# Performance work log

Measured on AMD Instinct MI355X. Metric: run time of the kernel, lower is better.

The kernel has to match this reference:

```python
import jax, jax.numpy as jnp
import numpy as np

B, C, H, W = 4, 64, 160, 160
COUT, K = 64, 3
STRIDE, PAD, DIL = 1, 1, 1


def setup_inputs() -> dict:
    key = jax.random.key(0)
    k1, k2, k3, k4, k5 = jax.random.split(key, 5)
    x = jax.random.normal(k1, (B, C, H, W), dtype=jnp.float32)
    # small offset-conv weights -> offsets of O(1) pixel, realistic sampling
    w_off = jax.random.normal(k2, (2 * K * K, C, K, K), dtype=jnp.float32) * 0.01
    b_off = jax.random.normal(k3, (2 * K * K,), dtype=jnp.float32) * 0.01
    weight = jax.random.normal(k4, (COUT, C, K, K), dtype=jnp.float32) / np.sqrt(C * K * K)
    bias = jax.random.normal(k5, (COUT,), dtype=jnp.float32) * 0.01
    return {"x": x, "w_off": w_off, "b_off": b_off, "weight": weight, "bias": bias}


def _deform_conv2d(x, offset, weight, bias):
    """torchvision-style deform_conv2d (v1, groups=1, offset_groups=1)."""
    b, c, h, w = x.shape
    cout, _, k, _ = weight.shape
    kk = k * k
    ho, wo = offset.shape[2], offset.shape[3]
    off = offset.reshape(b, kk, 2, ho, wo)
    dy, dx = off[:, :, 0], off[:, :, 1]  # [B,KK,Ho,Wo]
    # base sampling grid: p0 + kernel offset
    base_y = (jnp.arange(ho) * STRIDE - PAD)[None, :] + (jnp.arange(k) * DIL)[:, None]  # [K,Ho]
    base_x = (jnp.arange(wo) * STRIDE - PAD)[None, :] + (jnp.arange(k) * DIL)[:, None]  # [K,Wo]
    by = jnp.repeat(base_y, k, axis=0)   # [KK,Ho]  (k index = kh*K + kw)
    bx = jnp.tile(base_x, (k, 1))        # [KK,Wo]
    py = by[None, :, :, None] + dy       # [B,KK,Ho,Wo]
    px = bx[None, :, None, :] + dx
    y0 = jnp.floor(py)
    x0 = jnp.floor(px)
    ly = (py - y0)[:, None]              # [B,1,KK,Ho,Wo]
    lx = (px - x0)[:, None]
    y0i = y0.astype(jnp.int32)
    x0i = x0.astype(jnp.int32)
    x_flat = x.reshape(b, c, h * w)

    def gather(yi, xi):
        valid = (yi >= 0) & (yi < h) & (xi >= 0) & (xi < w)
        yc = jnp.clip(yi, 0, h - 1)
        xc = jnp.clip(xi, 0, w - 1)
        lin = (yc * w + xc).reshape(b, 1, -1)
        v = jnp.take_along_axis(x_flat, lin, axis=2).reshape(b, c, kk, ho, wo)
        return v * valid[:, None].astype(x.dtype)

    v00 = gather(y0i, x0i)
    v01 = gather(y0i, x0i + 1)
    v10 = gather(y0i + 1, x0i)
    v11 = gather(y0i + 1, x0i + 1)
    sampled = (v00 * (1 - ly) * (1 - lx) + v01 * (1 - ly) * lx
               + v10 * ly * (1 - lx) + v11 * ly * lx)  # [B,C,KK,Ho,Wo]
    out = jnp.einsum('bckhw,ock->bohw', sampled, weight.reshape(cout, c, kk))
    return out + bias[None, :, None, None]


def reference(x, w_off, b_off, weight, bias):
    offset = jax.lax.conv_general_dilated(
        x, w_off, (STRIDE, STRIDE), ((PAD, PAD), (PAD, PAD)),
        rhs_dilation=(DIL, DIL),
        dimension_numbers=('NCHW', 'OIHW', 'NCHW')) + b_off[None, :, None, None]
    return _deform_conv2d(x, offset, weight, bias)
```

## Files before the change

### kernel.cpp

```cpp
#include <hip/hip_runtime.h>
#include <hip/hip_bf16.h>

#define Bq   4
#define Cc   64
#define Hh   160
#define Ww   160
#define HWp  (Hh * Ww)
#define COUTc 64

typedef __attribute__((ext_vector_type(8))) _Float16 f16x8;
typedef __attribute__((ext_vector_type(4))) _Float16 f16x4;
typedef __attribute__((ext_vector_type(4))) float f32x4;
typedef __attribute__((ext_vector_type(2))) float f32x2;
typedef __attribute__((ext_vector_type(4))) int   int4v;

#define WTBF_SHORTS   (72 * 512)
#define WTOFFF_SHORTS (36 * 512)
#define XCL_OFS       (WTBF_SHORTS + WTOFFF_SHORTS)
#define XCL_PIX       ((size_t)Bq * HWp)
#define XCL_SHORTS    (XCL_PIX * 64 + 64)

#define HROWS 7
#define HCOLS 36
#define HPX   72
#define HSTR  (HCOLS * HPX)

__device__ __forceinline__ short f2h(float f) {
    union { _Float16 h; short s; } v; v.h = (_Float16)f; return v.s;
}
__device__ __forceinline__ unsigned pk2h(float a, float b) {
    union { _Float16 h[2]; unsigned u; } v;
    v.h[0] = (_Float16)a; v.h[1] = (_Float16)b; return v.u;
}
__device__ __forceinline__ f16x8 vsplat(_Float16 v) {
    return (f16x8){v, v, v, v, v, v, v, v};
}

__global__ __launch_bounds__(256) void prep_all(const float* __restrict__ x,
                                                const float* __restrict__ w,
                                                const float* __restrict__ w_off,
                                                short* __restrict__ ws) {
    int blk = blockIdx.x;
    int tid = threadIdx.x;
    if (blk < 400) {
        int g = blk * 256 + tid;
        int b = g / HWp, p = g - b * HWp;
        const float* xp = x + (size_t)b * Cc * HWp + p;
        short* op = ws + XCL_OFS + (size_t)g * 64;
#pragma unroll
        for (int cg = 0; cg < 8; ++cg) {
            unsigned d[4];
#pragma unroll
            for (int dj = 0; dj < 4; ++dj) {
                float f0 = xp[(size_t)(cg * 8 + 2 * dj) * HWp];
                float f1 = xp[(size_t)(cg * 8 + 2 * dj + 1) * HWp];
                d[dj] = pk2h(f0, f1);
            }
            *(int4v*)(op + cg * 8) = *(int4v*)d;
        }
    } else if (blk < 544) {
        int i = (blk - 400) * 256 + tid;
        if (i < WTBF_SHORTS) {
            int fidx = i >> 9, r = i & 511;
            int l = r >> 3, j = r & 7;
            int cg = fidx & 3, th = fidx >> 2;
            int tap = th >> 1, h = th & 1;
            int o = cg * 16 + (l & 15);
            int c = h * 32 + ((l >> 4) << 3) + j;
            ws[i] = f2h(w[o * 576 + c * 9 + tap]);
        }
        if (i < WTOFFF_SHORTS) {
            int fidx = i >> 9, r = i & 511;
            int l = r >> 3, j = r & 7;
            int g = fidx & 1, th = fidx >> 1;
            int tap = th >> 1, h = th & 1;
            int oc = g * 16 + (l & 15);
            int c = h * 32 + ((l >> 4) << 3) + j;
            float v = (oc < 18) ? w_off[oc * 576 + c * 9 + tap] : 0.f;
            ws[WTBF_SHORTS + i] = f2h(v);
        }
    } else {
        if (tid < 8)
            *(int4v*)((char*)(ws + XCL_OFS) + XCL_PIX * 128 + tid * 16) =
                (int4v){0, 0, 0, 0};
    }
}

__global__ __launch_bounds__(256, 3) void fused_cl(const short* __restrict__ ws,
                                                   const float* __restrict__ b_off,
                                                   const float* __restrict__ bias,
                                                   float* __restrict__ out) {
    __shared__ short halo_s[HROWS * HCOLS * HPX];
    __shared__ float offbuf[64][20];
    __shared__ int4v tapT[64][9];

    int tid = threadIdx.x;
    int wid = tid >> 6;
    int l   = tid & 63;
    int lr  = l & 15;
    int lg  = l >> 4;

    int bid = blockIdx.x;
    int g_blk = (bid & 7) * 200 + (bid >> 3);

    int b  = g_blk / 400;
    int r  = g_blk - b * 400;
    int ty2 = r / 5;
    int tx2 = r - ty2 * 5;
    int y  = ty2 * 2;
    int x0 = tx2 * 32;

    const short* wTbF   = ws;
    const short* wToffF = ws + WTBF_SHORTS;
    const char*  xclb   = (const char*)(ws + XCL_OFS) + (size_t)b * HWp * 128;

    for (int i = tid; i < HROWS * HCOLS * 8; i += 256) {
        int pl = i >> 3, cg2 = i & 7;
        int hy = pl / HCOLS, hx = pl - hy * HCOLS;
        int gy = y - 2 + hy, gx = x0 - 2 + hx;
        int4v v;
        if (gy >= 0 && gy < Hh && gx >= 0 && gx < Ww)
            v = *(const int4v*)(xclb + (size_t)(gy * Ww + gx) * 128 + cg2 * 16);
        else
            v = (int4v){0, 0, 0, 0};
        *(int4v*)(halo_s + pl * HPX + cg2 * 8) = v;
    }
    __syncthreads();

    {
        int rowoff = wid >> 1;
        int colw   = (wid & 1) * 16 + lr;
        int hxb    = colw + 1;
        int hoffA[9];
#pragma unroll
        for (int t = 0; t < 9; ++t) {
            int ty = t / 3, tx = t - ty * 3;
            hoffA[t] = (rowoff + ty + 1) * HSTR + (hxb + tx) * HPX + lg * 8;
        }
        const short* wofr = wToffF + l * 8;
        f32x4 accO0 = {0.f, 0.f, 0.f, 0.f};
        f32x4 accO1 = {0.f, 0.f, 0.f, 0.f};
        f16x8 sB0[4], sB1[4];
#pragma unroll
        for (int u = 0; u < 4; ++u) {
            sB0[u] = *(const f16x8*)(wofr + u * 1024);
            sB1[u] = *(const f16x8*)(wofr + u * 1024 + 512);
        }
        f16x8 sa2[2];
        sa2[0] = *(const f16x8*)(halo_s + hoffA[0]);
#pragma unroll
        for (int u = 0; u < 18; ++u) {
            const int s4 = u & 3;
            if (u + 1 < 18) {
                const int t2 = (u + 1) >> 1, h2 = (u + 1) & 1;
                sa2[(u + 1) & 1] = *(const f16x8*)(halo_s + hoffA[t2] + h2 * 32);
            }
            accO0 = __builtin_amdgcn_mfma_f32_16x16x32_f16(sa2[u & 1], sB0[s4], accO0, 0, 0, 0);
            accO1 = __builtin_amdgcn_mfma_f32_16x16x32_f16(sa2[u & 1], sB1[s4], accO1, 0, 0, 0);
            if (u + 4 < 18) {
                sB0[s4] = *(const f16x8*)(wofr + (u + 4) * 1024);
                sB1[s4] = *(const f16x8*)(wofr + (u + 4) * 1024 + 512);
            }
            __builtin_amdgcn_sched_barrier(0);
        }
        float bv0 = b_off[lr];
#pragma unroll
        for (int j = 0; j < 4; ++j)
            offbuf[wid * 16 + lg * 4 + j][lr] = accO0[j] + bv0;
        if (lr < 2) {
            float bv1 = b_off[16 + lr];
#pragma unroll
            for (int j = 0; j < 4; ++j)
                offbuf[wid * 16 + lg * 4 + j][16 + lr] = accO1[j] + bv1;
        }
    }
    __syncthreads();

    for (int i = tid; i < 576; i += 256) {
        int px = i / 9, tap = i - px * 9;
        int prow = px >> 5, pcol = px & 31;
        int ty = tap / 3, tx = tap - ty * 3;
        f32x2 d2 = *(const f32x2*)&offbuf[px][2 * tap];
        float py  = (float)(y + prow - 1 + ty) + d2[0];
        float pxf = (float)(x0 + pcol - 1 + tx) + d2[1];
        float fy = floorf(py), fx = floorf(pxf);
        float ly = py - fy, lx = pxf - fx;
        int iy0 = (int)fy, ix0 = (int)fx;
        int iy1 = iy0 + 1, ix1 = ix0 + 1;
        bool vy0 = (iy0 >= 0) && (iy0 < Hh);
        bool vy1 = (iy1 >= 0) && (iy1 < Hh);
        bool vx0 = (ix0 >= 0) && (ix0 < Ww);
        bool vx1 = (ix1 >= 0) && (ix1 < Ww);
        float w00 = (vy0 && vx0) ? (1.f - ly) * (1.f - lx) : 0.f;
        float w01 = (vy0 && vx1) ? (1.f - ly) * lx         : 0.f;
        float w10 = (vy1 && vx0) ? ly * (1.f - lx)         : 0.f;
        float w11 = (vy1 && vx1) ? ly * lx                 : 0.f;
        int hy = iy0 - (y - 2);
        int hx = ix0 - (x0 - 2);
        bool inH = (hy >= 0) && (hy <= HROWS - 2) && (hx >= 0) && (hx <= HCOLS - 2);
        union { f16x4 h4; int iw[2]; } wu;
        wu.h4 = (f16x4){(_Float16)w00, (_Float16)w01,
                        (_Float16)w10, (_Float16)w11};
        int4v tv;
        tv[0] = inH ? (hy * HSTR + hx * HPX) : -1;
        tv[1] = (iy0 & 0xffff) | (ix0 << 16);
        tv[2] = wu.iw[0];
        tv[3] = wu.iw[1];
        tapT[px][tap] = tv;
    }
    __syncthreads();

    f32x4 acc[4];
#pragma unroll
    for (int cg = 0; cg < 4; ++cg) acc[cg] = (f32x4){0.f, 0.f, 0.f, 0.f};
    int px3 = wid * 16 + lr;
    const short* wfb = wTbF + l * 8;

    f16x8 sBc[2][4];
#pragma unroll
    for (int cg = 0; cg < 4; ++cg) {
        sBc[0][cg] = *(const f16x8*)(wfb + (0 * 4 + cg) * 512);
        sBc[1][cg] = *(const f16x8*)(wfb + (1 * 4 + cg) * 512);
    }

    int4v tp[2];
    tp[0] = tapT[px3][0];
    tp[1] = tapT[px3][1];

    f16x8 cst[2][8];
    {
        const short* q = halo_s + max(tp[0][0], 0) + lg * 8;
#pragma unroll
        for (int h = 0; h < 2; ++h) {
            const short* qh = q + h * 32;
            cst[0][h * 4 + 0] = *(const f16x8*)(qh);
            cst[0][h * 4 + 1] = *(const f16x8*)(qh + HPX);
            cst[0][h * 4 + 2] = *(const f16x8*)(qh + HSTR);
            cst[0][h * 4 + 3] = *(const f16x8*)(qh + HSTR + HPX);
        }
    }

#pragma unroll
    for (int t = 0; t < 9; ++t) {
        const int cur = t & 1, nx = cur ^ 1;

        const int ho = tp[cur][0];
        const int fb = tp[cur][1];
        union { int iw[2]; f16x4 h4; } wu;
        wu.iw[0] = tp[cur][2];
        wu.iw[1] = tp[cur][3];
        f16x4 wg = wu.h4;

        if (t + 2 < 9)
            tp[cur] = tapT[px3][t + 2];

        if (t < 8) {
            const short* q = halo_s + max(tp[nx][0], 0) + lg * 8;
#pragma unroll
            for (int h = 0; h < 2; ++h) {
                const short* qh = q + h * 32;
                cst[nx][h * 4 + 0] = *(const f16x8*)(qh);
                cst[nx][h * 4 + 1] = *(const f16x8*)(qh + HPX);
                cst[nx][h * 4 + 2] = *(const f16x8*)(qh + HSTR);
                cst[nx][h * 4 + 3] = *(const f16x8*)(qh + HSTR + HPX);
            }
        }
        __builtin_amdgcn_sched_barrier(0);

#pragma unroll
        for (int h = 0; h < 2; ++h) {
            const int u = 2 * t + h, s = u & 1;
            f16x8 a = cst[cur][h * 4 + 0] * vsplat(wg[0])
                    + cst[cur][h * 4 + 1] * vsplat(wg[1])
                    + cst[cur][h * 4 + 2] * vsplat(wg[2])
                    + cst[cur][h * 4 + 3] * vsplat(wg[3]);
            if (ho < 0) {
                int iy0 = (int)(short)(fb & 0xffff);
                int ix0 = fb >> 16;
                int cy0 = min(max(iy0, 0), Hh - 1), cy1 = min(max(iy0 + 1, 0), Hh - 1);
                int cx0 = min(max(ix0, 0), Ww - 1), cx1 = min(max(ix0 + 1, 0), Ww - 1);
                int cbh = h * 64 + lg * 16;
                f16x8 g00 = *(const f16x8*)(xclb + (size_t)(cy0 * Ww + cx0) * 128 + cbh);
                f16x8 g01 = *(const f16x8*)(xclb + (size_t)(cy0 * Ww + cx1) * 128 + cbh);
                f16x8 g10 = *(const f16x8*)(xclb + (size_t)(cy1 * Ww + cx0) * 128 + cbh);
                f16x8 g11 = *(const f16x8*)(xclb + (size_t)(cy1 * Ww + cx1) * 128 + cbh);
                a = g00 * vsplat(wg[0]) + g01 * vsplat(wg[1])
                  + g10 * vsplat(wg[2]) + g11 * vsplat(wg[3]);
            }
            acc[0] = __builtin_amdgcn_mfma_f32_16x16x32_f16(a, sBc[s][0], acc[0], 0, 0, 0);
            acc[1] = __builtin_amdgcn_mfma_f32_16x16x32_f16(a, sBc[s][1], acc[1], 0, 0, 0);
            acc[2] = __builtin_amdgcn_mfma_f32_16x16x32_f16(a, sBc[s][2], acc[2], 0, 0, 0);
            acc[3] = __builtin_amdgcn_mfma_f32_16x16x32_f16(a, sBc[s][3], acc[3], 0, 0, 0);
            if (u + 2 < 18) {
#pragma unroll
                for (int cg = 0; cg < 4; ++cg)
                    sBc[s][cg] = *(const f16x8*)(wfb + ((u + 2) * 4 + cg) * 512);
            }
        }
        __builtin_amdgcn_sched_barrier(0);
    }

    float* obase = out + (size_t)b * COUTc * HWp + y * Ww + x0;
#pragma unroll
    for (int cg = 0; cg < 4; ++cg) {
        int o = cg * 16 + lr;
        float bv = bias[o];
#pragma unroll
        for (int j = 0; j < 4; ++j) {
            int px = wid * 16 + lg * 4 + j;
            int prow = px >> 5, pcol = px & 31;
            obase[(size_t)o * HWp + prow * Ww + pcol] = acc[cg][j] + bv;
        }
    }
}

extern "C" void kernel_launch(void* const* d_in, const int* in_sizes, int n_in,
                              void* d_out, int out_size, void* d_ws, size_t ws_size,
                              hipStream_t stream) {
    const float* x      = (const float*)d_in[0];
    const float* w_off  = (const float*)d_in[1];
    const float* b_off  = (const float*)d_in[2];
    const float* weight = (const float*)d_in[3];
    const float* bias   = (const float*)d_in[4];
    float* outp = (float*)d_out;
    short* ws   = (short*)d_ws;

    prep_all<<<545, 256, 0, stream>>>(x, weight, w_off, ws);

    int nblocks = (Bq * HWp) / 64;
    fused_cl<<<nblocks, 256, 0, stream>>>(ws, b_off, bias, outp);
}
```

Measured before the change: 49.65 us.

## Compute tap tables in registers, shrink halo to raise occupancy

Each lane now computes its own bilinear tap offsets and weights into register arrays. This replaces the shared-memory tapT table, the cooperative fill loop and one barrier. The halo tile drops from 7 to 6 rows and launch bounds go from 3 to 4 blocks per CU, lowering LDS use so more blocks fit. The cost is that each lane repeats the tap math for its pixel across the 4 lane groups, register pressure rises, and more taps fall outside the smaller halo and take the slower global-gather fallback, which now recomputes coordinates from offbuf.

```diff
diff --git a/kernel.cpp b/kernel.cpp
--- a/kernel.cpp
+++ b/kernel.cpp
@@ -20,7 +20,7 @@
 #define XCL_PIX       ((size_t)Bq * HWp)
 #define XCL_SHORTS    (XCL_PIX * 64 + 64)
 
-#define HROWS 7
+#define HROWS 6
 #define HCOLS 36
 #define HPX   72
 #define HSTR  (HCOLS * HPX)
@@ -86,13 +86,12 @@
     }
 }
 
-__global__ __launch_bounds__(256, 3) void fused_cl(const short* __restrict__ ws,
+__global__ __launch_bounds__(256, 4) void fused_cl(const short* __restrict__ ws,
                                                    const float* __restrict__ b_off,
                                                    const float* __restrict__ bias,
                                                    float* __restrict__ out) {
     __shared__ short halo_s[HROWS * HCOLS * HPX];
     __shared__ float offbuf[64][20];
-    __shared__ int4v tapT[64][9];
 
     int tid = threadIdx.x;
     int wid = tid >> 6;
@@ -176,11 +175,14 @@
     }
     __syncthreads();
 
-    for (int i = tid; i < 576; i += 256) {
-        int px = i / 9, tap = i - px * 9;
-        int prow = px >> 5, pcol = px & 31;
-        int ty = tap / 3, tx = tap - ty * 3;
-        f32x2 d2 = *(const f32x2*)&offbuf[px][2 * tap];
+    int px3 = wid * 16 + lr;
+    int prow = px3 >> 5, pcol = px3 & 31;
+    int   hoT[9];
+    f16x4 wgT[9];
+#pragma unroll
+    for (int t = 0; t < 9; ++t) {
+        int ty = t / 3, tx = t - ty * 3;
+        f32x2 d2 = *(const f32x2*)&offbuf[px3][2 * t];
         float py  = (float)(y + prow - 1 + ty) + d2[0];
         float pxf = (float)(x0 + pcol - 1 + tx) + d2[1];
         float fy = floorf(py), fx = floorf(pxf);
@@ -198,22 +200,14 @@
         int hy = iy0 - (y - 2);
         int hx = ix0 - (x0 - 2);
         bool inH = (hy >= 0) && (hy <= HROWS - 2) && (hx >= 0) && (hx <= HCOLS - 2);
-        union { f16x4 h4; int iw[2]; } wu;
-        wu.h4 = (f16x4){(_Float16)w00, (_Float16)w01,
-                        (_Float16)w10, (_Float16)w11};
-        int4v tv;
-        tv[0] = inH ? (hy * HSTR + hx * HPX) : -1;
-        tv[1] = (iy0 & 0xffff) | (ix0 << 16);
-        tv[2] = wu.iw[0];
-        tv[3] = wu.iw[1];
-        tapT[px][tap] = tv;
-    }
-    __syncthreads();
+        hoT[t] = inH ? (hy * HSTR + hx * HPX) : -1;
+        wgT[t] = (f16x4){(_Float16)w00, (_Float16)w01,
+                         (_Float16)w10, (_Float16)w11};
+    }
 
     f32x4 acc[4];
 #pragma unroll
     for (int cg = 0; cg < 4; ++cg) acc[cg] = (f32x4){0.f, 0.f, 0.f, 0.f};
-    int px3 = wid * 16 + lr;
     const short* wfb = wTbF + l * 8;
 
     f16x8 sBc[2][4];
@@ -223,13 +217,9 @@
         sBc[1][cg] = *(const f16x8*)(wfb + (1 * 4 + cg) * 512);
     }
 
-    int4v tp[2];
-    tp[0] = tapT[px3][0];
-    tp[1] = tapT[px3][1];
-
     f16x8 cst[2][8];
     {
-        const short* q = halo_s + max(tp[0][0], 0) + lg * 8;
+        const short* q = halo_s + max(hoT[0], 0) + lg * 8;
 #pragma unroll
         for (int h = 0; h < 2; ++h) {
             const short* qh = q + h * 32;
@@ -243,19 +233,11 @@
 #pragma unroll
     for (int t = 0; t < 9; ++t) {
         const int cur = t & 1, nx = cur ^ 1;
-
-        const int ho = tp[cur][0];
-        const int fb = tp[cur][1];
-        union { int iw[2]; f16x4 h4; } wu;
-        wu.iw[0] = tp[cur][2];
-        wu.iw[1] = tp[cur][3];
-        f16x4 wg = wu.h4;
-
-        if (t + 2 < 9)
-            tp[cur] = tapT[px3][t + 2];
+        const int ho = hoT[t];
+        f16x4 wg = wgT[t];
 
         if (t < 8) {
-            const short* q = halo_s + max(tp[nx][0], 0) + lg * 8;
+            const short* q = halo_s + max(hoT[t + 1], 0) + lg * 8;
 #pragma unroll
             for (int h = 0; h < 2; ++h) {
                 const short* qh = q + h * 32;
@@ -275,8 +257,11 @@
                     + cst[cur][h * 4 + 2] * vsplat(wg[2])
                     + cst[cur][h * 4 + 3] * vsplat(wg[3]);
             if (ho < 0) {
-                int iy0 = (int)(short)(fb & 0xffff);
-                int ix0 = fb >> 16;
+                int ty_ = t / 3, tx_ = t - ty_ * 3;
+                f32x2 d2 = *(const f32x2*)&offbuf[px3][2 * t];
+                float py  = (float)(y + prow - 1 + ty_) + d2[0];
+                float pxf = (float)(x0 + pcol - 1 + tx_) + d2[1];
+                int iy0 = (int)floorf(py), ix0 = (int)floorf(pxf);
                 int cy0 = min(max(iy0, 0), Hh - 1), cy1 = min(max(iy0 + 1, 0), Hh - 1);
                 int cx0 = min(max(ix0, 0), Ww - 1), cx1 = min(max(ix0 + 1, 0), Ww - 1);
                 int cbh = h * 64 + lg * 16;
@@ -308,8 +293,8 @@
 #pragma unroll
         for (int j = 0; j < 4; ++j) {
             int px = wid * 16 + lg * 4 + j;
-            int prow = px >> 5, pcol = px & 31;
-            obase[(size_t)o * HWp + prow * Ww + pcol] = acc[cg][j] + bv;
+            int prw = px >> 5, pcl = px & 31;
+            obase[(size_t)o * HWp + prw * Ww + pcl] = acc[cg][j] + bv;
         }
     }
 }
```

Measured after the change: 80.44 us. +62.0%, slower.
